# Kernel tuning notes

Hardware: AMD Instinct MI355X
Metric: run time of the kernel (lower is better)

## Reference

```python
import jax, jax.numpy as jnp
import numpy as np

N, T, F = 64, 256, 13          # nodes/frame, frames, node features
E = N * (N - 1)                 # complete directed graph (as in _extract_graph)
P, HID, HEADS = 128, 128, 4     # pooling_channels, hidden_dim, attention_heads


def setup_inputs() -> dict:
    key = jax.random.key(0)
    ks = jax.random.split(key, 32)
    s = 0.05
    src, dst = np.nonzero(~np.eye(N, dtype=bool))
    edge_index = jnp.array(np.stack([src, dst]), dtype=jnp.int32)
    C1 = P // HEADS
    rn = lambda k, shp: jax.random.normal(k, shp, jnp.float32) * s
    return {
        "x": jax.random.normal(ks[0], (T, N, F), jnp.float32),
        "edge_index": edge_index,
        "edge_attr": jax.random.uniform(ks[1], (T, E, 1), jnp.float32),
        # GATConv 1: in=F, heads=4, per-head C1, edge_dim=1, concat -> P
        "W1": rn(ks[2], (F, P)),
        "a_src1": rn(ks[3], (HEADS, C1)),
        "a_dst1": rn(ks[4], (HEADS, C1)),
        "We1": rn(ks[5], (1, P)),
        "a_edge1": rn(ks[6], (HEADS, C1)),
        "b1": jnp.zeros((P,), jnp.float32),
        # GATConv 2: in=P, heads=1, out=HID
        "W2": rn(ks[7], (P, HID)),
        "a_src2": rn(ks[8], (1, HID)),
        "a_dst2": rn(ks[9], (1, HID)),
        "We2": rn(ks[10], (1, HID)),
        "a_edge2": rn(ks[11], (1, HID)),
        "b2": jnp.zeros((HID,), jnp.float32),
        # AttentionalAggregation gate: Linear(HID, 1)
        "Wg": rn(ks[12], (HID, 1)),
        "bg": jnp.zeros((1,), jnp.float32),
        # bidirectional LSTM: input 2*HID, hidden HID (torch gate order i,f,g,o)
        "Wih_f": rn(ks[13], (4 * HID, 2 * HID)),
        "Whh_f": rn(ks[14], (4 * HID, HID)),
        "bih_f": jnp.zeros((4 * HID,), jnp.float32),
        "bhh_f": jnp.zeros((4 * HID,), jnp.float32),
        "Wih_b": rn(ks[15], (4 * HID, 2 * HID)),
        "Whh_b": rn(ks[16], (4 * HID, HID)),
        "bih_b": jnp.zeros((4 * HID,), jnp.float32),
        "bhh_b": jnp.zeros((4 * HID,), jnp.float32),
        # output layer: Linear(2*HID, 1)
        "Wo": rn(ks[17], (2 * HID, 1)),
        "bo": jnp.zeros((1,), jnp.float32),
    }


def reference(x, edge_index, edge_attr, W1, a_src1, a_dst1, We1, a_edge1, b1,
              W2, a_src2, a_dst2, We2, a_edge2, b2, Wg, bg,
              Wih_f, Whh_f, bih_f, bhh_f, Wih_b, Whh_b, bih_b, bhh_b, Wo, bo):
    n = x.shape[1]
    src, dst = edge_index[0], edge_index[1]

    def gat(h_in, ea, W, a_s, a_d, We, a_e, b):
        # PyG GATConv with edge_dim, add_self_loops=False, eval (no dropout)
        heads = a_s.shape[0]
        hc = W.shape[1]
        c = hc // heads
        h = (h_in @ W).reshape(-1, heads, c)          # [N, H, C]
        e = (ea @ We).reshape(-1, heads, c)           # [E, H, C]
        alpha = (h * a_s).sum(-1)[src] + (h * a_d).sum(-1)[dst] + (e * a_e).sum(-1)
        alpha = jax.nn.leaky_relu(alpha, 0.2)         # [E, H]
        amax = jax.ops.segment_max(alpha, dst, num_segments=n)
        amax = jnp.where(jnp.isfinite(amax), amax, 0.0)
        ex = jnp.exp(alpha - amax[dst])
        den = jax.ops.segment_sum(ex, dst, num_segments=n)
        coef = ex / (den[dst] + 1e-16)                # softmax per dst node
        out = jax.ops.segment_sum(h[src] * coef[:, :, None], dst, num_segments=n)
        return out.reshape(n, hc) + b

    def gnn(xt, eat):
        h1 = jax.nn.relu(gat(xt, eat, W1, a_src1, a_dst1, We1, a_edge1, b1))
        h2 = jax.nn.relu(gat(h1, eat, W2, a_src2, a_dst2, We2, a_edge2, b2))
        attn = jax.nn.softmax(h2 @ Wg + bg, axis=0)   # AttentionalAggregation
        return jnp.concatenate([(attn * h2).sum(0), h2.max(0)])  # [2*HID]

    embs = jax.vmap(gnn)(x, edge_attr)                # [T, 2*HID]

    def lstm(Wih, Whh, bih, bhh, seq):
        hid = Whh.shape[1]
        def step(carry, xt):
            h, c = carry
            g = xt @ Wih.T + h @ Whh.T + bih + bhh
            i, f, gg, o = jnp.split(g, 4)
            c = jax.nn.sigmoid(f) * c + jax.nn.sigmoid(i) * jnp.tanh(gg)
            h = jax.nn.sigmoid(o) * jnp.tanh(c)
            return (h, c), h
        init = (jnp.zeros((hid,), seq.dtype), jnp.zeros((hid,), seq.dtype))
        _, outs = jax.lax.scan(step, init, seq)
        return outs

    outs_f = lstm(Wih_f, Whh_f, bih_f, bhh_f, embs)
    outs_b = lstm(Wih_b, Whh_b, bih_b, bhh_b, embs[::-1])
    # lstm_out[:, -1, :] = [fwd state at t=T-1, bwd state at t=T-1]
    last = jnp.concatenate([outs_f[-1], outs_b[0]])
    return jax.nn.sigmoid(last @ Wo + bo)[None, :]    # [1, 1]
```

## Files before the change

kernel.cpp:

```cpp
#include <hip/hip_runtime.h>
#include <math.h>

#define NN 64
#define TT 256
#define FF 13
#define EE 4032
#define PP 128
#define HH 128

typedef float f32x4 __attribute__((ext_vector_type(4)));
typedef _Float16 f16x2 __attribute__((ext_vector_type(2)));

__device__ __forceinline__ float wave_sum64(float v) {
#pragma unroll
  for (int off = 32; off > 0; off >>= 1) v += __shfl_xor(v, off, 64);
  return v;
}
__device__ __forceinline__ float sigm(float x) { return 1.f / (1.f + __expf(-x)); }
__device__ __forceinline__ float tanh_fast(float x) { return 1.f - 2.f / (__expf(2.f * x) + 1.f); }

#define ROTF(x, N) __builtin_bit_cast(float, __builtin_amdgcn_mov_dpp( \
    __builtin_bit_cast(int, x), 0x120 + (N), 0xF, 0xF, true))
__device__ __forceinline__ float rdlane(float v, int l) {
  return __builtin_bit_cast(float, __builtin_amdgcn_readlane(__builtin_bit_cast(int, v), l));
}
__device__ __forceinline__ float allred_max(float v) {
  v = fmaxf(v, ROTF(v, 1)); v = fmaxf(v, ROTF(v, 2));
  v = fmaxf(v, ROTF(v, 4)); v = fmaxf(v, ROTF(v, 8));
  return fmaxf(fmaxf(rdlane(v, 0), rdlane(v, 16)),
               fmaxf(rdlane(v, 32), rdlane(v, 48)));
}
__device__ __forceinline__ float allred_sum(float v) {
  v += ROTF(v, 1); v += ROTF(v, 2); v += ROTF(v, 4); v += ROTF(v, 8);
  return (rdlane(v, 0) + rdlane(v, 16)) + (rdlane(v, 32) + rdlane(v, 48));
}

__device__ __forceinline__ unsigned pk_f16(float lo, float hi) {
  unsigned u;
  asm("v_cvt_pkrtz_f16_f32 %0, %1, %2" : "=v"(u) : "v"(lo), "v"(hi));
  return u;
}
__device__ __forceinline__ float fdot2u(unsigned h, unsigned w, float acc) {
#if __has_builtin(__builtin_amdgcn_fdot2)
  return __builtin_amdgcn_fdot2(__builtin_bit_cast(f16x2, h),
                                __builtin_bit_cast(f16x2, w), acc, false);
#else
  const f16x2 a = __builtin_bit_cast(f16x2, h);
  const f16x2 b = __builtin_bit_cast(f16x2, w);
  return acc + (float)a.x * (float)b.x + (float)a.y * (float)b.y;
#endif
}
__device__ __forceinline__ float ror1(float x) {
  return __builtin_bit_cast(float, __builtin_amdgcn_mov_dpp(
      __builtin_bit_cast(int, x), 0x121, 0xF, 0xF, true));
}
__device__ __forceinline__ float qswap1(float x) {
  return __builtin_bit_cast(float, __builtin_amdgcn_mov_dpp(
      __builtin_bit_cast(int, x), 0xB1, 0xF, 0xF, true));
}

__global__ __launch_bounds__(512, 2)
void gnn_kernel(const float* __restrict__ x, const float* __restrict__ ea_g,
                const float* __restrict__ W1, const float* __restrict__ a_src1,
                const float* __restrict__ a_dst1, const float* __restrict__ We1,
                const float* __restrict__ a_edge1, const float* __restrict__ b1,
                const float* __restrict__ W2, const float* __restrict__ a_src2,
                const float* __restrict__ a_dst2, const float* __restrict__ We2,
                const float* __restrict__ a_edge2, const float* __restrict__ b2,
                const float* __restrict__ Wg, const float* __restrict__ bg,
                float* __restrict__ embs)
{
  __shared__ float x_s[NN * FF];
  __shared__ float W1_s[FF * PP];
  __shared__ float ea_s[EE];
  __shared__ float hA_s[NN * PP];
  __shared__ float hB_s[NN * PP];
  __shared__ float as1_s[4 * NN];
  __shared__ float ad1_s[4 * NN];
  __shared__ float asrc1_s[PP], adst1_s[PP], asrc2_s[PP], adst2_s[PP];
  __shared__ float b1_s[PP], b2_s[PP], Wg_s[PP];
  __shared__ float as2_s[NN], ad2_s[NN];
  __shared__ __align__(16) float coefA_s[16 * 272];
  __shared__ float denA_s[16 * 4];
  __shared__ __align__(16) float coefB_s[16 * 68];
  __shared__ float denB_s[16];
  __shared__ float wed_s[8];
  __shared__ float attn_s[NN];

  const int tid = threadIdx.x;
  const int t = blockIdx.x;
  const int wave = tid >> 6, lane = tid & 63;

  for (int i = tid; i < NN * FF; i += 512) x_s[i] = x[t * NN * FF + i];
  for (int i = tid; i < FF * PP; i += 512) W1_s[i] = W1[i];
  for (int i = tid; i < EE; i += 512) ea_s[i] = ea_g[t * EE + i];
  if (tid < PP) {
    asrc1_s[tid] = a_src1[tid]; adst1_s[tid] = a_dst1[tid];
    asrc2_s[tid] = a_src2[tid]; adst2_s[tid] = a_dst2[tid];
    b1_s[tid] = b1[tid]; b2_s[tid] = b2[tid]; Wg_s[tid] = Wg[tid];
  }
  if (tid >= 128 && tid < 132) {
    const int h = tid - 128;
    float acc = 0.f;
    for (int c = 0; c < 32; ++c) acc += We1[h * 32 + c] * a_edge1[h * 32 + c];
    wed_s[h] = acc;
  }
  if (tid == 132) {
    float acc = 0.f;
    for (int c = 0; c < 128; ++c) acc += We2[c] * a_edge2[c];
    wed_s[4] = acc;
  }
  __syncthreads();

  {
    const int c = tid & 127, ib = tid >> 7;
    for (int q = 0; q < 16; ++q) {
      const int i = ib * 16 + q;
      float acc = 0.f;
#pragma unroll
      for (int f = 0; f < FF; ++f) acc += x_s[i * FF + f] * W1_s[f * PP + c];
      hA_s[i * PP + c] = acc;
    }
  }
  __syncthreads();

  {
    const int half = tid >> 8;
    const int tt2 = tid & 255;
    const int i = tt2 >> 2, h = tt2 & 3;
    const float* aw = half ? adst1_s : asrc1_s;
    float acc = 0.f;
    for (int cc = 0; cc < 32; ++cc) {
      const int c = (cc + tid) & 31;
      acc += hA_s[i * PP + h * 32 + c] * aw[h * 32 + c];
    }
    if (half) ad1_s[h * 64 + i] = acc; else as1_s[h * 64 + i] = acc;
  }
  __syncthreads();

  for (int g = 0; g < 4; ++g) {
#pragma unroll
    for (int r = 0; r < 2; ++r) {
      const int d = g * 16 + r * 8 + wave;
      const int dl = d & 15;
      float a0, a1, a2, a3;
      if (lane != d) {
        const int jj = lane * 63 + (d < lane ? d : d - 1);
        const float ev = ea_s[jj];
        a0 = as1_s[0 * 64 + lane] + ad1_s[0 * 64 + d] + ev * wed_s[0];
        a1 = as1_s[1 * 64 + lane] + ad1_s[1 * 64 + d] + ev * wed_s[1];
        a2 = as1_s[2 * 64 + lane] + ad1_s[2 * 64 + d] + ev * wed_s[2];
        a3 = as1_s[3 * 64 + lane] + ad1_s[3 * 64 + d] + ev * wed_s[3];
        a0 = a0 > 0.f ? a0 : 0.2f * a0;
        a1 = a1 > 0.f ? a1 : 0.2f * a1;
        a2 = a2 > 0.f ? a2 : 0.2f * a2;
        a3 = a3 > 0.f ? a3 : 0.2f * a3;
      } else { a0 = a1 = a2 = a3 = -1e30f; }
      const float m0 = allred_max(a0), m1 = allred_max(a1);
      const float m2 = allred_max(a2), m3 = allred_max(a3);
      const float p0 = (lane != d) ? __expf(a0 - m0) : 0.f;
      const float p1 = (lane != d) ? __expf(a1 - m1) : 0.f;
      const float p2 = (lane != d) ? __expf(a2 - m2) : 0.f;
      const float p3 = (lane != d) ? __expf(a3 - m3) : 0.f;
      const float s0 = allred_sum(p0), s1 = allred_sum(p1);
      const float s2 = allred_sum(p2), s3 = allred_sum(p3);
      coefA_s[dl * 272 + 0 * 68 + lane] = p0;
      coefA_s[dl * 272 + 1 * 68 + lane] = p1;
      coefA_s[dl * 272 + 2 * 68 + lane] = p2;
      coefA_s[dl * 272 + 3 * 68 + lane] = p3;
      if (lane == 0) {
        denA_s[dl * 4 + 0] = s0; denA_s[dl * 4 + 1] = s1;
        denA_s[dl * 4 + 2] = s2; denA_s[dl * 4 + 3] = s3;
      }
    }
    __syncthreads();
    {
      const int half = lane >> 5;
      const int dl = wave * 2 + half;
      const int d  = g * 16 + dl;
      const int c0 = (lane & 31) * 4;
      const int hh = c0 >> 5;
      const float* cfb = &coefA_s[dl * 272 + hh * 68];
      float ac0 = 0.f, ac1 = 0.f, ac2 = 0.f, ac3 = 0.f;
#pragma unroll 4
      for (int s = 0; s < 64; s += 4) {
        const float4 cf = *(const float4*)&cfb[s];
        const float4 h0 = *(const float4*)&hA_s[(s + 0) * PP + c0];
        ac0 += cf.x * h0.x; ac1 += cf.x * h0.y; ac2 += cf.x * h0.z; ac3 += cf.x * h0.w;
        const float4 h1v = *(const float4*)&hA_s[(s + 1) * PP + c0];
        ac0 += cf.y * h1v.x; ac1 += cf.y * h1v.y; ac2 += cf.y * h1v.z; ac3 += cf.y * h1v.w;
        const float4 h2v = *(const float4*)&hA_s[(s + 2) * PP + c0];
        ac0 += cf.z * h2v.x; ac1 += cf.z * h2v.y; ac2 += cf.z * h2v.z; ac3 += cf.z * h2v.w;
        const float4 h3v = *(const float4*)&hA_s[(s + 3) * PP + c0];
        ac0 += cf.w * h3v.x; ac1 += cf.w * h3v.y; ac2 += cf.w * h3v.z; ac3 += cf.w * h3v.w;
      }
      const float inv = 1.f / (denA_s[dl * 4 + hh] + 1e-16f);
      const float4 bv = *(const float4*)&b1_s[c0];
      float4 o;
      o.x = fmaxf(ac0 * inv + bv.x, 0.f);
      o.y = fmaxf(ac1 * inv + bv.y, 0.f);
      o.z = fmaxf(ac2 * inv + bv.z, 0.f);
      o.w = fmaxf(ac3 * inv + bv.w, 0.f);
      *(float4*)&hB_s[d * PP + c0] = o;
    }
    __syncthreads();
  }

  {
    const int cg = tid & 31, ig = tid >> 5;
    const int c0 = cg * 4, i0 = ig * 4;
    float acc[4][4];
#pragma unroll
    for (int ii = 0; ii < 4; ++ii)
#pragma unroll
      for (int cc = 0; cc < 4; ++cc) acc[ii][cc] = 0.f;
    for (int f0 = 0; f0 < 128; f0 += 4) {
      float4 wv0 = *(const float4*)&W2[(f0 + 0) * PP + c0];
      float4 wv1 = *(const float4*)&W2[(f0 + 1) * PP + c0];
      float4 wv2 = *(const float4*)&W2[(f0 + 2) * PP + c0];
      float4 wv3 = *(const float4*)&W2[(f0 + 3) * PP + c0];
#pragma unroll
      for (int ii = 0; ii < 4; ++ii) {
        const float4 hv = *(const float4*)&hB_s[(i0 + ii) * PP + f0];
        acc[ii][0] += hv.x * wv0.x + hv.y * wv1.x + hv.z * wv2.x + hv.w * wv3.x;
        acc[ii][1] += hv.x * wv0.y + hv.y * wv1.y + hv.z * wv2.y + hv.w * wv3.y;
        acc[ii][2] += hv.x * wv0.z + hv.y * wv1.z + hv.z * wv2.z + hv.w * wv3.z;
        acc[ii][3] += hv.x * wv0.w + hv.y * wv1.w + hv.z * wv2.w + hv.w * wv3.w;
      }
    }
#pragma unroll
    for (int ii = 0; ii < 4; ++ii) {
      float4 o; o.x = acc[ii][0]; o.y = acc[ii][1]; o.z = acc[ii][2]; o.w = acc[ii][3];
      *(float4*)&hA_s[(i0 + ii) * PP + c0] = o;
    }
  }
  __syncthreads();

  if (tid < 128) {
    const int i = tid >> 1, sel = tid & 1;
    const float* aw = sel ? adst2_s : asrc2_s;
    float acc = 0.f;
    for (int cc = 0; cc < 128; ++cc) {
      const int c = (cc + tid) & 127;
      acc += hA_s[i * PP + c] * aw[c];
    }
    if (sel) ad2_s[i] = acc; else as2_s[i] = acc;
  }
  __syncthreads();

  for (int g = 0; g < 4; ++g) {
#pragma unroll
    for (int r = 0; r < 2; ++r) {
      const int d = g * 16 + r * 8 + wave;
      const int dl = d & 15;
      float a;
      if (lane != d) {
        const int jj = lane * 63 + (d < lane ? d : d - 1);
        a = as2_s[lane] + ad2_s[d] + ea_s[jj] * wed_s[4];
        a = a > 0.f ? a : 0.2f * a;
      } else a = -1e30f;
      const float m = allred_max(a);
      const float p = (lane != d) ? __expf(a - m) : 0.f;
      const float ssum = allred_sum(p);
      coefB_s[dl * 68 + lane] = p;
      if (lane == 0) denB_s[dl] = ssum;
    }
    __syncthreads();
    {
      const int half = lane >> 5;
      const int dl = wave * 2 + half;
      const int d  = g * 16 + dl;
      const int c0 = (lane & 31) * 4;
      const float* cfb = &coefB_s[dl * 68];
      float ac0 = 0.f, ac1 = 0.f, ac2 = 0.f, ac3 = 0.f;
#pragma unroll 4
      for (int s = 0; s < 64; s += 4) {
        const float4 cf = *(const float4*)&cfb[s];
        const float4 h0 = *(const float4*)&hA_s[(s + 0) * PP + c0];
        ac0 += cf.x * h0.x; ac1 += cf.x * h0.y; ac2 += cf.x * h0.z; ac3 += cf.x * h0.w;
        const float4 h1v = *(const float4*)&hA_s[(s + 1) * PP + c0];
        ac0 += cf.y * h1v.x; ac1 += cf.y * h1v.y; ac2 += cf.y * h1v.z; ac3 += cf.y * h1v.w;
        const float4 h2v = *(const float4*)&hA_s[(s + 2) * PP + c0];
        ac0 += cf.z * h2v.x; ac1 += cf.z * h2v.y; ac2 += cf.z * h2v.z; ac3 += cf.z * h2v.w;
        const float4 h3v = *(const float4*)&hA_s[(s + 3) * PP + c0];
        ac0 += cf.w * h3v.x; ac1 += cf.w * h3v.y; ac2 += cf.w * h3v.z; ac3 += cf.w * h3v.w;
      }
      const float inv = 1.f / (denB_s[dl] + 1e-16f);
      const float4 bv = *(const float4*)&b2_s[c0];
      float4 o;
      o.x = fmaxf(ac0 * inv + bv.x, 0.f);
      o.y = fmaxf(ac1 * inv + bv.y, 0.f);
      o.z = fmaxf(ac2 * inv + bv.z, 0.f);
      o.w = fmaxf(ac3 * inv + bv.w, 0.f);
      *(float4*)&hB_s[d * PP + c0] = o;
    }
    __syncthreads();
  }

  if (tid < 64) {
    float acc = 0.f;
    for (int cc = 0; cc < 128; ++cc) {
      const int c = (cc + tid) & 127;
      acc += hB_s[tid * PP + c] * Wg_s[c];
    }
    const float logit = acc + bg[0];
    const float m = allred_max(logit);
    const float p = __expf(logit - m);
    const float ssum = allred_sum(p);
    attn_s[tid] = p / ssum;
  }
  __syncthreads();
  if (tid < 128) {
    const int c = tid;
    float acc = 0.f, mx = -1e30f;
    for (int i = 0; i < NN; ++i) {
      const float v = hB_s[i * PP + c];
      acc += attn_s[i] * v;
      mx = fmaxf(mx, v);
    }
    embs[t * 256 + c] = acc;
    embs[t * 256 + 128 + c] = mx;
  }
}

__global__ __launch_bounds__(512, 2)
void zproj_kernel(const float* __restrict__ embs,
                  const float* __restrict__ Wih_f, const float* __restrict__ bih_f,
                  const float* __restrict__ bhh_f,
                  const float* __restrict__ Wih_b, const float* __restrict__ bih_b,
                  const float* __restrict__ bhh_b,
                  float* __restrict__ Z, float* __restrict__ Zb)
{
  __shared__ float e_s[256];
  const int t = blockIdx.x;
  const int j = threadIdx.x;
  const bool bwd = (t == TT);
  const int tsrc = bwd ? (TT - 1) : t;
  if (j < 256) e_s[j] = embs[tsrc * 256 + j];
  __syncthreads();
  const float* W = bwd ? Wih_b : Wih_f;
  float acc = bwd ? (bih_b[j] + bhh_b[j]) : (bih_f[j] + bhh_f[j]);
  const float4* Wr = (const float4*)(W + j * 256);
  const float4* er = (const float4*)e_s;
#pragma unroll 8
  for (int k = 0; k < 64; ++k) {
    const float4 w = Wr[k];
    const float4 e = er[k];
    acc += w.x * e.x + w.y * e.y + w.z * e.z + w.w * e.w;
  }
  if (bwd) Zb[j] = acc; else Z[t * 512 + j] = acc;
}

__global__ __launch_bounds__(1024)
void lstm_kernel(const float* __restrict__ Z, const float* __restrict__ Zb,
                 const float* __restrict__ Whh_f,
                 const float* __restrict__ Wo, const float* __restrict__ bo,
                 float* __restrict__ out)
{
  __shared__ float h_s[128];
  __shared__ __align__(16) unsigned h16_s[64];
  __shared__ float p_s[1024];
  __shared__ float hb_s[128];
  __shared__ float red_s[16];
  const int tid = threadIdx.x;
  const int j = tid & 511;
  const int s = tid >> 9;
  const int m = tid & 15;
  const int j0 = j & ~15;

  const float* wbase = Whh_f + s * 64 + 4 * m;
#define LWR(r) \
  unsigned wa##r, wb##r; { \
    const float4 v = *(const float4*)(wbase + (j0 + ((m - (r)) & 15)) * 128); \
    wa##r = pk_f16(v.x, v.y); wb##r = pk_f16(v.z, v.w); }
  LWR(0)  LWR(1)  LWR(2)  LWR(3)  LWR(4)  LWR(5)  LWR(6)  LWR(7)
  LWR(8)  LWR(9)  LWR(10) LWR(11) LWR(12) LWR(13) LWR(14) LWR(15)
#undef LWR
  asm volatile("" : "+v"(wa0),  "+v"(wb0),  "+v"(wa1),  "+v"(wb1),
                    "+v"(wa2),  "+v"(wb2),  "+v"(wa3),  "+v"(wb3),
                    "+v"(wa4),  "+v"(wb4),  "+v"(wa5),  "+v"(wb5),
                    "+v"(wa6),  "+v"(wb6),  "+v"(wa7),  "+v"(wb7));
  asm volatile("" : "+v"(wa8),  "+v"(wb8),  "+v"(wa9),  "+v"(wb9),
                    "+v"(wa10), "+v"(wb10), "+v"(wa11), "+v"(wb11),
                    "+v"(wa12), "+v"(wb12), "+v"(wa13), "+v"(wb13),
                    "+v"(wa14), "+v"(wb14), "+v"(wa15), "+v"(wb15));

  float c = 0.f;
  if (tid < 128) h_s[tid] = 0.f;
  if (tid < 64) h16_s[tid] = 0u;
  __syncthreads();

  float zcur = (s == 0) ? Z[j] : 0.f;
  for (int t = 0; t < TT; ++t) {
    const float znext = (s == 0 && t < TT - 1) ? Z[(t + 1) * 512 + j] : 0.f;
    const uint2 hd = *(const uint2*)&h16_s[s * 32 + 2 * m];
    float acc = 0.f;
#define STEP(r) \
    acc = fdot2u(hd.x, wa##r, acc); \
    acc = fdot2u(hd.y, wb##r, acc); \
    acc = ror1(acc);
    STEP(0)  STEP(1)  STEP(2)  STEP(3)  STEP(4)  STEP(5)  STEP(6)  STEP(7)
    STEP(8)  STEP(9)  STEP(10) STEP(11) STEP(12) STEP(13) STEP(14) STEP(15)
#undef STEP
    p_s[tid] = acc + zcur;
    __syncthreads();
    if (tid < 128) {
      const float gi = p_s[tid]       + p_s[512 + tid];
      const float gf = p_s[128 + tid] + p_s[640 + tid];
      const float gg = p_s[256 + tid] + p_s[768 + tid];
      const float go = p_s[384 + tid] + p_s[896 + tid];
      c = sigm(gf) * c + sigm(gi) * tanh_fast(gg);
      const float hnew = sigm(go) * tanh_fast(c);
      h_s[tid] = hnew;
      const float hnb = qswap1(hnew);
      if (!(tid & 1)) h16_s[tid >> 1] = pk_f16(hnew, hnb);
    }
    __syncthreads();
    zcur = znext;
  }

  if (tid < 128) {
    const float gi = Zb[tid], gg = Zb[256 + tid], go = Zb[384 + tid];
    const float cb = sigm(gi) * tanh_fast(gg);
    hb_s[tid] = sigm(go) * tanh_fast(cb);
  }
  __syncthreads();

  float v = 0.f;
  if (tid < 128) v = h_s[tid] * Wo[tid];
  else if (tid < 256) v = hb_s[tid - 128] * Wo[tid];
  v = wave_sum64(v);
  if ((tid & 63) == 0) red_s[tid >> 6] = v;
  __syncthreads();
  if (tid == 0) {
    float sum = bo[0];
#pragma unroll
    for (int k = 0; k < 16; ++k) sum += red_s[k];
    out[0] = 1.f / (1.f + __expf(-sum));
  }
}

extern "C" void kernel_launch(void* const* d_in, const int* in_sizes, int n_in,
                              void* d_out, int out_size, void* d_ws, size_t ws_size,
                              hipStream_t stream) {
  const float* x       = (const float*)d_in[0];
  const float* ea      = (const float*)d_in[2];
  const float* W1      = (const float*)d_in[3];
  const float* a_src1  = (const float*)d_in[4];
  const float* a_dst1  = (const float*)d_in[5];
  const float* We1     = (const float*)d_in[6];
  const float* a_edge1 = (const float*)d_in[7];
  const float* b1      = (const float*)d_in[8];
  const float* W2      = (const float*)d_in[9];
  const float* a_src2  = (const float*)d_in[10];
  const float* a_dst2  = (const float*)d_in[11];
  const float* We2     = (const float*)d_in[12];
  const float* a_edge2 = (const float*)d_in[13];
  const float* b2      = (const float*)d_in[14];
  const float* Wg      = (const float*)d_in[15];
  const float* bg      = (const float*)d_in[16];
  const float* Wih_f   = (const float*)d_in[17];
  const float* Whh_f   = (const float*)d_in[18];
  const float* bih_f   = (const float*)d_in[19];
  const float* bhh_f   = (const float*)d_in[20];
  const float* Wih_b   = (const float*)d_in[21];
  const float* bih_b   = (const float*)d_in[23];
  const float* bhh_b   = (const float*)d_in[24];
  const float* Wo      = (const float*)d_in[25];
  const float* bo      = (const float*)d_in[26];
  float* out = (float*)d_out;

  float* embs = (float*)d_ws;
  float* Z    = embs + 256 * 256;
  float* Zb   = Z + 256 * 512;

  gnn_kernel<<<256, 512, 0, stream>>>(x, ea, W1, a_src1, a_dst1, We1, a_edge1, b1,
                                      W2, a_src2, a_dst2, We2, a_edge2, b2, Wg, bg, embs);
  zproj_kernel<<<257, 512, 0, stream>>>(embs, Wih_f, bih_f, bhh_f, Wih_b, bih_b, bhh_b, Z, Zb);
  lstm_kernel<<<1, 1024, 0, stream>>>(Z, Zb, Whh_f, Wo, bo, out);
}
```

Baseline: 260.4 us.

## Compute LSTM recurrent matvec with bf16 MFMA and gate-interleaved Z layout

Replaces the per-lane fdot2 plus DPP-rotate recurrent matvec with bf16 16x16x32 MFMA instructions. Whh rows are permuted so each MFMA output column holds the four gates of one hidden unit. The input-projection kernel writes Z in a gate-interleaved layout so each thread loads all four gate preactivations with one float4, and h is double-buffered in LDS so each step needs only one barrier instead of two. The changes aim to shorten the serial per-timestep critical path, at the cost of lower bf16 precision in place of fp16 and redundant gate math across the lanes of each 16-lane group.

```diff
diff --git a/kernel.cpp b/kernel.cpp
--- a/kernel.cpp
+++ b/kernel.cpp
@@ -9,7 +9,8 @@
 #define HH 128
 
 typedef float f32x4 __attribute__((ext_vector_type(4)));
-typedef _Float16 f16x2 __attribute__((ext_vector_type(2)));
+typedef short s16x8 __attribute__((ext_vector_type(8)));
+typedef unsigned u32x4 __attribute__((ext_vector_type(4)));
 
 __device__ __forceinline__ float wave_sum64(float v) {
 #pragma unroll
@@ -35,28 +36,12 @@
   return (rdlane(v, 0) + rdlane(v, 16)) + (rdlane(v, 32) + rdlane(v, 48));
 }
 
-__device__ __forceinline__ unsigned pk_f16(float lo, float hi) {
-  unsigned u;
-  asm("v_cvt_pkrtz_f16_f32 %0, %1, %2" : "=v"(u) : "v"(lo), "v"(hi));
-  return u;
-}
-__device__ __forceinline__ float fdot2u(unsigned h, unsigned w, float acc) {
-#if __has_builtin(__builtin_amdgcn_fdot2)
-  return __builtin_amdgcn_fdot2(__builtin_bit_cast(f16x2, h),
-                                __builtin_bit_cast(f16x2, w), acc, false);
-#else
-  const f16x2 a = __builtin_bit_cast(f16x2, h);
-  const f16x2 b = __builtin_bit_cast(f16x2, w);
-  return acc + (float)a.x * (float)b.x + (float)a.y * (float)b.y;
-#endif
-}
-__device__ __forceinline__ float ror1(float x) {
-  return __builtin_bit_cast(float, __builtin_amdgcn_mov_dpp(
-      __builtin_bit_cast(int, x), 0x121, 0xF, 0xF, true));
-}
-__device__ __forceinline__ float qswap1(float x) {
-  return __builtin_bit_cast(float, __builtin_amdgcn_mov_dpp(
-      __builtin_bit_cast(int, x), 0xB1, 0xF, 0xF, true));
+__device__ __forceinline__ unsigned bf16rne(float x) {
+  const unsigned u = __builtin_bit_cast(unsigned, x);
+  return (u + 0x7FFFu + ((u >> 16) & 1u)) >> 16;
+}
+__device__ __forceinline__ unsigned pk_bf16(float lo, float hi) {
+  return bf16rne(lo) | (bf16rne(hi) << 16);
 }
 
 __global__ __launch_bounds__(512, 2)
@@ -348,76 +333,87 @@
     const float4 e = er[k];
     acc += w.x * e.x + w.y * e.y + w.z * e.z + w.w * e.w;
   }
-  if (bwd) Zb[j] = acc; else Z[t * 512 + j] = acc;
+  if (bwd) Zb[j] = acc;
+  else     Z[t * 512 + (j & 127) * 4 + (j >> 7)] = acc;
 }
 
 __global__ __launch_bounds__(1024)
-void lstm_kernel(const float* __restrict__ Z, const float* __restrict__ Zb,
+void lstm_kernel(const float* __restrict__ Zt, const float* __restrict__ Zb,
                  const float* __restrict__ Whh_f,
                  const float* __restrict__ Wo, const float* __restrict__ bo,
                  float* __restrict__ out)
 {
+  __shared__ __align__(16) unsigned h16_s[2][64];
   __shared__ float h_s[128];
-  __shared__ __align__(16) unsigned h16_s[64];
-  __shared__ float p_s[1024];
   __shared__ float hb_s[128];
   __shared__ float red_s[16];
   const int tid = threadIdx.x;
-  const int j = tid & 511;
-  const int s = tid >> 9;
-  const int m = tid & 15;
-  const int j0 = j & ~15;
-
-  const float* wbase = Whh_f + s * 64 + 4 * m;
-#define LWR(r) \
-  unsigned wa##r, wb##r; { \
-    const float4 v = *(const float4*)(wbase + (j0 + ((m - (r)) & 15)) * 128); \
-    wa##r = pk_f16(v.x, v.y); wb##r = pk_f16(v.z, v.w); }
-  LWR(0)  LWR(1)  LWR(2)  LWR(3)  LWR(4)  LWR(5)  LWR(6)  LWR(7)
-  LWR(8)  LWR(9)  LWR(10) LWR(11) LWR(12) LWR(13) LWR(14) LWR(15)
-#undef LWR
-  asm volatile("" : "+v"(wa0),  "+v"(wb0),  "+v"(wa1),  "+v"(wb1),
-                    "+v"(wa2),  "+v"(wb2),  "+v"(wa3),  "+v"(wb3),
-                    "+v"(wa4),  "+v"(wb4),  "+v"(wa5),  "+v"(wb5),
-                    "+v"(wa6),  "+v"(wb6),  "+v"(wa7),  "+v"(wb7));
-  asm volatile("" : "+v"(wa8),  "+v"(wb8),  "+v"(wa9),  "+v"(wb9),
-                    "+v"(wa10), "+v"(wb10), "+v"(wa11), "+v"(wb11),
-                    "+v"(wa12), "+v"(wb12), "+v"(wa13), "+v"(wb13),
-                    "+v"(wa14), "+v"(wb14), "+v"(wa15), "+v"(wb15));
-
-  float c = 0.f;
-  if (tid < 128) h_s[tid] = 0.f;
-  if (tid < 64) h16_s[tid] = 0u;
-  __syncthreads();
-
-  float zcur = (s == 0) ? Z[j] : 0.f;
+  const int wave = tid >> 6, lane = tid & 63;
+  const int g16 = lane >> 4;
+  const int p_  = lane & 15;
+  const int u0 = wave * 8 + g16;
+  const int u1 = u0 + 4;
+  const int rowT0 = (p_ & 3) * 128 + wave * 8 + 0 + (p_ >> 2);
+  const int rowT1 = (p_ & 3) * 128 + wave * 8 + 4 + (p_ >> 2);
+  const float* rp0 = Whh_f + rowT0 * 128;
+  const float* rp1 = Whh_f + rowT1 * 128;
+
+#define LDW(nm, rp, q) \
+  unsigned nm##x, nm##y, nm##z, nm##w; { \
+    const float4 va = *(const float4*)&(rp)[(q) * 32 + g16 * 8]; \
+    const float4 vb = *(const float4*)&(rp)[(q) * 32 + g16 * 8 + 4]; \
+    nm##x = pk_bf16(va.x, va.y); nm##y = pk_bf16(va.z, va.w); \
+    nm##z = pk_bf16(vb.x, vb.y); nm##w = pk_bf16(vb.z, vb.w); }
+  LDW(a00, rp0, 0) LDW(a01, rp0, 1) LDW(a02, rp0, 2) LDW(a03, rp0, 3)
+  LDW(a10, rp1, 0) LDW(a11, rp1, 1) LDW(a12, rp1, 2) LDW(a13, rp1, 3)
+#undef LDW
+  asm volatile("" : "+v"(a00x), "+v"(a00y), "+v"(a00z), "+v"(a00w),
+                    "+v"(a01x), "+v"(a01y), "+v"(a01z), "+v"(a01w),
+                    "+v"(a02x), "+v"(a02y), "+v"(a02z), "+v"(a02w),
+                    "+v"(a03x), "+v"(a03y), "+v"(a03z), "+v"(a03w));
+  asm volatile("" : "+v"(a10x), "+v"(a10y), "+v"(a10z), "+v"(a10w),
+                    "+v"(a11x), "+v"(a11y), "+v"(a11z), "+v"(a11w),
+                    "+v"(a12x), "+v"(a12y), "+v"(a12z), "+v"(a12w),
+                    "+v"(a13x), "+v"(a13y), "+v"(a13z), "+v"(a13w));
+
+  float c0 = 0.f, c1 = 0.f, h0 = 0.f, h1 = 0.f;
+  if (tid < 64) { h16_s[0][tid] = 0u; h16_s[1][tid] = 0u; }
+  __syncthreads();
+
+#define MKA(nm) __builtin_bit_cast(s16x8, (u32x4){nm##x, nm##y, nm##z, nm##w})
+  int pb = 0;
   for (int t = 0; t < TT; ++t) {
-    const float znext = (s == 0 && t < TT - 1) ? Z[(t + 1) * 512 + j] : 0.f;
-    const uint2 hd = *(const uint2*)&h16_s[s * 32 + 2 * m];
-    float acc = 0.f;
-#define STEP(r) \
-    acc = fdot2u(hd.x, wa##r, acc); \
-    acc = fdot2u(hd.y, wb##r, acc); \
-    acc = ror1(acc);
-    STEP(0)  STEP(1)  STEP(2)  STEP(3)  STEP(4)  STEP(5)  STEP(6)  STEP(7)
-    STEP(8)  STEP(9)  STEP(10) STEP(11) STEP(12) STEP(13) STEP(14) STEP(15)
-#undef STEP
-    p_s[tid] = acc + zcur;
+    const float4 z0 = *(const float4*)&Zt[t * 512 + u0 * 4];
+    const float4 z1 = *(const float4*)&Zt[t * 512 + u1 * 4];
+    const u32x4 b0 = *(const u32x4*)&h16_s[pb][ 0 + g16 * 4];
+    const u32x4 b1 = *(const u32x4*)&h16_s[pb][16 + g16 * 4];
+    const u32x4 b2 = *(const u32x4*)&h16_s[pb][32 + g16 * 4];
+    const u32x4 b3 = *(const u32x4*)&h16_s[pb][48 + g16 * 4];
+    f32x4 acc0 = {0.f, 0.f, 0.f, 0.f}, acc1 = {0.f, 0.f, 0.f, 0.f};
+#define MM(A, B, C) C = __builtin_amdgcn_mfma_f32_16x16x32_bf16( \
+    (A), __builtin_bit_cast(s16x8, B), C, 0, 0, 0)
+    MM(MKA(a00), b0, acc0); MM(MKA(a10), b0, acc1);
+    MM(MKA(a01), b1, acc0); MM(MKA(a11), b1, acc1);
+    MM(MKA(a02), b2, acc0); MM(MKA(a12), b2, acc1);
+    MM(MKA(a03), b3, acc0); MM(MKA(a13), b3, acc1);
+#undef MM
+    const float i0 = sigm(acc0.x + z0.x), f0 = sigm(acc0.y + z0.y);
+    const float g0 = tanh_fast(acc0.z + z0.z), o0 = sigm(acc0.w + z0.w);
+    c0 = f0 * c0 + i0 * g0; h0 = o0 * tanh_fast(c0);
+    const float i1 = sigm(acc1.x + z1.x), f1 = sigm(acc1.y + z1.y);
+    const float g1 = tanh_fast(acc1.z + z1.z), o1 = sigm(acc1.w + z1.w);
+    c1 = f1 * c1 + i1 * g1; h1 = o1 * tanh_fast(c1);
+    if (p_ == 0) {
+      unsigned short* hp = (unsigned short*)&h16_s[pb ^ 1][0];
+      hp[u0] = (unsigned short)bf16rne(h0);
+      hp[u1] = (unsigned short)bf16rne(h1);
+    }
     __syncthreads();
-    if (tid < 128) {
-      const float gi = p_s[tid]       + p_s[512 + tid];
-      const float gf = p_s[128 + tid] + p_s[640 + tid];
-      const float gg = p_s[256 + tid] + p_s[768 + tid];
-      const float go = p_s[384 + tid] + p_s[896 + tid];
-      c = sigm(gf) * c + sigm(gi) * tanh_fast(gg);
-      const float hnew = sigm(go) * tanh_fast(c);
-      h_s[tid] = hnew;
-      const float hnb = qswap1(hnew);
-      if (!(tid & 1)) h16_s[tid >> 1] = pk_f16(hnew, hnb);
-    }
-    __syncthreads();
-    zcur = znext;
-  }
+    pb ^= 1;
+  }
+#undef MKA
+
+  if (p_ == 0) { h_s[u0] = h0; h_s[u1] = h1; }
 
   if (tid < 128) {
     const float gi = Zb[tid], gg = Zb[256 + tid], go = Zb[384 + tid];
```

Measured after the change: 475.6 us. +82.6%, slower.
